# Optimization experiments

Measured on AMD Instinct MI355X. Metric: run time of the kernel, lower is better.

The kernel has to match this reference:

```python
import jax, jax.numpy as jnp
import numpy as np

N_HEAD = 16
QMIN, QMAX = 0.0, 255.0  # 8-bit asymmetric


def fake_quantize(x, scale, zp):
    # LearnableFakeQuantize (asymmetric, 8-bit) with straight-through round.
    q = x / scale + zp
    q = q + jax.lax.stop_gradient(jnp.round(q) - q)  # STE round
    q = jnp.clip(q, QMIN, QMAX)
    return (q - zp) * scale


def setup_inputs() -> dict:
    key = jax.random.key(0)
    ks = jax.random.split(key, 4)
    B, T, C = 2, 2048, 1024
    return {
        "hidden_states": jax.random.normal(ks[0], (B, T, C), jnp.float32),
        "W_attn": jax.random.normal(ks[1], (C, 3 * C), jnp.float32) * (1.0 / np.sqrt(C)),
        "b_attn": jnp.zeros((3 * C,), jnp.float32),
        "W_proj": jax.random.normal(ks[2], (C, C), jnp.float32) * (1.0 / np.sqrt(C)),
        "b_proj": jnp.zeros((C,), jnp.float32),
        "kv_scale": jnp.full((1,), 0.05, jnp.float32),
        "kv_zp": jnp.full((1,), 128.0, jnp.float32),
    }


def reference(hidden_states, W_attn, b_attn, W_proj, b_proj, kv_scale, kv_zp):
    B, T, C = hidden_states.shape
    H = N_HEAD
    D = C // H
    qkv = hidden_states @ W_attn + b_attn            # [B,T,3C]
    q, k, v = jnp.split(qkv, 3, axis=2)
    # [B,T,C] -> [B,H,T,D]
    q = q.reshape(B, T, H, D).transpose(0, 2, 1, 3)
    k = k.reshape(B, T, H, D).transpose(0, 2, 1, 3)
    v = v.reshape(B, T, H, D).transpose(0, 2, 1, 3)
    k = fake_quantize(k, kv_scale, kv_zp)
    v = fake_quantize(v, kv_scale, kv_zp)
    scores = jnp.einsum("bhqd,bhkd->bhqk", q, k) / jnp.sqrt(jnp.asarray(D, q.dtype))
    causal = jnp.tril(jnp.ones((T, T), bool))        # bias[:T,:T]
    scores = jnp.where(causal, scores, jnp.asarray(-jnp.inf, scores.dtype))
    attn = jax.nn.softmax(scores, axis=-1)
    out = jnp.einsum("bhqk,bhkd->bhqd", attn, v)     # [B,H,T,D]
    out = out.transpose(0, 2, 1, 3).reshape(B, T, C)
    return out @ W_proj + b_proj
```

## Files before the change

kernel.cpp:

```cpp
#include <hip/hip_runtime.h>
#include <math.h>

#define TB 2048
#define CC 1024
#define NH 16
#define HD 64

typedef __bf16 bf16x8 __attribute__((ext_vector_type(8)));
typedef __bf16 bf16x4 __attribute__((ext_vector_type(4)));
typedef float  f32x4  __attribute__((ext_vector_type(4)));

__device__ inline float exp2fast(float x) { return __builtin_amdgcn_exp2f(x); }

__device__ __forceinline__ void gl_lds16(const __bf16* g, __bf16* l) {
    __builtin_amdgcn_global_load_lds(
        (const __attribute__((address_space(1))) void*)g,
        (__attribute__((address_space(3))) void*)l, 16, 0, 0);
}

__global__ __launch_bounds__(256)
void prep_kernel(const float* __restrict__ hidden, __bf16* __restrict__ hb,
                 const float* __restrict__ Wa, __bf16* __restrict__ wat,
                 const float* __restrict__ Wp, __bf16* __restrict__ wpt)
{
    __shared__ __bf16 L[64][68];
    const int tid = threadIdx.x;
    const int bid = blockIdx.x;
    if (bid < 4096) {
        int i = (bid * 256 + tid) * 4;
        f32x4 v = *(const f32x4*)&hidden[i];
        bf16x4 o;
        o.x = (__bf16)v.x; o.y = (__bf16)v.y; o.z = (__bf16)v.z; o.w = (__bf16)v.w;
        *(bf16x4*)&hb[i] = o;
        return;
    }
    const float* src; __bf16* dst; int N, n0, k0;
    if (bid < 4096 + 768) {
        int t = bid - 4096;
        src = Wa; dst = wat; N = 3072;
        n0 = (t % 48) * 64; k0 = (t / 48) * 64;
    } else {
        int t = bid - 4864;
        src = Wp; dst = wpt; N = 1024;
        n0 = (t % 16) * 64; k0 = (t / 16) * 64;
    }
    #pragma unroll
    for (int i = 0; i < 4; i++) {
        int id = tid + i * 256;
        int r = id >> 4, c = (id & 15) * 4;
        f32x4 v = *(const f32x4*)&src[(size_t)(k0 + r) * N + n0 + c];
        bf16x4 o;
        o.x = (__bf16)v.x; o.y = (__bf16)v.y; o.z = (__bf16)v.z; o.w = (__bf16)v.w;
        *(bf16x4*)&L[r][c] = o;
    }
    __syncthreads();
    #pragma unroll
    for (int i = 0; i < 4; i++) {
        int id = tid + i * 256;
        int nr = id >> 4, kc = (id & 15) * 4;
        bf16x4 o;
        o.x = L[kc + 0][nr]; o.y = L[kc + 1][nr];
        o.z = L[kc + 2][nr]; o.w = L[kc + 3][nr];
        *(bf16x4*)&dst[(size_t)(n0 + nr) * 1024 + k0 + kc] = o;
    }
}

template<int BN, int MODE>
__global__ __launch_bounds__(256)
void gemm_bt(const __bf16* __restrict__ A, const __bf16* __restrict__ Bt,
             const float* __restrict__ bias,
             __bf16* __restrict__ o0, __bf16* __restrict__ o1,
             __bf16* __restrict__ o2, float* __restrict__ of,
             int M, int N, int K,
             const float* __restrict__ scp, const float* __restrict__ zpp)
{
    constexpr int NT = BN / 32;
    __shared__ __bf16 Asm[128][64];
    __shared__ __bf16 Bsm[BN][64];

    const int tid  = threadIdx.x;
    const int m0   = blockIdx.y * 128;
    const int n0   = blockIdx.x * BN;
    const int w    = tid >> 6, lane = tid & 63;
    const int wm   = (w & 1) * 64, wn = (w >> 1) * (BN / 2);
    const int r16  = lane & 15, quad = lane >> 4;
    const int srow = lane >> 3;
    const int scol = ((lane & 7) ^ srow) * 8;
    const int rsw  = r16 & 7;

    f32x4 acc[NT][4];
    #pragma unroll
    for (int i = 0; i < NT; i++)
        #pragma unroll
        for (int j = 0; j < 4; j++) acc[i][j] = 0.f;

    for (int k0 = 0; k0 < K; k0 += 64) {
        #pragma unroll
        for (int p = 0; p < 4; p++)
            gl_lds16(&A[(size_t)(m0 + w * 32 + p * 8 + srow) * K + k0 + scol],
                     &Asm[w * 32 + p * 8][0]);
        #pragma unroll
        for (int p = 0; p < BN / 32; p++)
            gl_lds16(&Bt[(size_t)(n0 + w * (BN / 4) + p * 8 + srow) * K + k0 + scol],
                     &Bsm[w * (BN / 4) + p * 8][0]);
        __syncthreads();

        #pragma unroll
        for (int ks = 0; ks < 2; ks++) {
            const int col = ((ks * 4 + quad) ^ rsw) * 8;
            bf16x8 af[4], bfr[NT];
            #pragma unroll
            for (int mt = 0; mt < 4; mt++)
                af[mt] = *(const bf16x8*)&Asm[wm + mt * 16 + r16][col];
            #pragma unroll
            for (int nt = 0; nt < NT; nt++)
                bfr[nt] = *(const bf16x8*)&Bsm[wn + nt * 16 + r16][col];
            #pragma unroll
            for (int nt = 0; nt < NT; nt++)
                #pragma unroll
                for (int mt = 0; mt < 4; mt++)
                    acc[nt][mt] = __builtin_amdgcn_mfma_f32_16x16x32_bf16(
                        bfr[nt], af[mt], acc[nt][mt], 0, 0, 0);
        }
        __syncthreads();
    }

    const float sc = scp[0];
    const float zp = zpp[0];

    #pragma unroll
    for (int nt = 0; nt < NT; nt++) {
        #pragma unroll
        for (int mt = 0; mt < 4; mt++) {
            int gm = m0 + wm + mt * 16 + r16;
            int gn = n0 + wn + nt * 16 + quad * 4;
            f32x4 val = acc[nt][mt] + *(const f32x4*)&bias[gn];
            if (MODE == 1) {
                *(f32x4*)&of[(size_t)gm * N + gn] = val;
            } else {
                int part = gn >> 10;
                int idx  = gn & 1023;
                int h = idx >> 6, d = idx & 63;
                int b = gm >> 11, t = gm & 2047;
                if (part == 0) {
                    size_t off = (((size_t)(b * NH + h)) * TB + t) * HD + d;
                    bf16x4 st;
                    #pragma unroll
                    for (int r = 0; r < 4; r++)
                        st[r] = (__bf16)(val[r] * 0.18033688f);
                    *(bf16x4*)&o0[off] = st;
                } else if (part == 1) {
                    size_t off = (((size_t)(b * NH + h)) * TB + t) * HD + d;
                    bf16x4 st;
                    #pragma unroll
                    for (int r = 0; r < 4; r++) {
                        float qv = val[r] / sc + zp;
                        qv = rintf(qv);
                        qv = fminf(fmaxf(qv, 0.f), 255.f);
                        st[r] = (__bf16)((qv - zp) * sc);
                    }
                    *(bf16x4*)&o1[off] = st;
                } else {
                    #pragma unroll
                    for (int r = 0; r < 4; r++) {
                        float qv = val[r] / sc + zp;
                        qv = rintf(qv);
                        qv = fminf(fmaxf(qv, 0.f), 255.f);
                        size_t offT = (((size_t)(b * NH + h)) * HD + d + r) * TB + t;
                        o2[offT] = (__bf16)((qv - zp) * sc);
                    }
                }
            }
        }
    }
}

__global__ __launch_bounds__(512, 4)
void attn_mfma(const __bf16* __restrict__ Q, const __bf16* __restrict__ Kg,
               const __bf16* __restrict__ VgT, __bf16* __restrict__ O)
{
    __shared__ alignas(16) __bf16 Ksm[2][64][64];
    __shared__ alignas(16) __bf16 Vsm[2][64][64];

    const int tid  = threadIdx.x;
    const int p    = blockIdx.x >> 5;
    const int bh   = blockIdx.x & 31;
    const int w    = tid >> 6, lane = tid & 63;
    const int wq   = w & 3;
    const int qt   = (w < 4) ? (31 - p) : p;
    const int ktmax = 31 - p;
    const int q0   = qt * 64;
    const int l15  = lane & 15, quad = lane >> 4;
    const int b    = bh >> 4, h = bh & 15;

    const int srow = tid >> 3;
    const int ssw  = ((tid & 7) ^ ((srow & 3) | (((srow >> 3) & 1) << 2))) * 8;

    const __bf16* Kbh = Kg  + (size_t)bh * TB * HD;
    const __bf16* Vbh = VgT + (size_t)bh * HD * TB;

    const __bf16* Qrow = Q + ((size_t)bh * TB + q0 + wq * 16 + l15) * HD;
    bf16x8 qf0 = *(const bf16x8*)&Qrow[quad * 8];
    bf16x8 qf1 = *(const bf16x8*)&Qrow[32 + quad * 8];

    const int rbase = (l15 >> 2) * 8 + (l15 & 3);
    const int fk   = (l15 & 3) | (((l15 >> 2) & 1) << 2);
    const int fv   = (l15 & 3) | (((l15 >> 3) & 1) << 2);
    const int kc0  = (quad ^ fk) * 8, kc1 = ((quad + 4) ^ fk) * 8;
    const int vc0  = (quad ^ fv) * 8, vc1 = ((quad + 4) ^ fv) * 8;

    bf16x8 af_l;
    {
        __bf16 v = (l15 == 0) ? (__bf16)1.0f : (__bf16)0.0f;
        #pragma unroll
        for (int j = 0; j < 8; j++) af_l[j] = v;
    }

    f32x4 acc_o[4], acc_l;
    #pragma unroll
    for (int nt = 0; nt < 4; nt++) acc_o[nt] = 0.f;
    acc_l = 0.f;
    float mrun = -3.0e38f;

    auto stage = [&](int buf, int kt) {
        gl_lds16(&Kbh[(size_t)(kt * 64 + srow) * HD + ssw], &Ksm[buf][w * 8][0]);
        gl_lds16(&Vbh[(size_t)srow * TB + kt * 64 + ssw],   &Vsm[buf][w * 8][0]);
    };

    stage(0, 0);
    __syncthreads();

    for (int kt = 0; kt <= ktmax; kt++) {
        const int cur = kt & 1;

        if (kt < ktmax) stage(cur ^ 1, kt + 1);

        if (kt <= qt) {
            const bool diag = (kt == qt);

            f32x4 s[4];
            #pragma unroll
            for (int nt = 0; nt < 4; nt++) s[nt] = 0.f;
            __builtin_amdgcn_s_setprio(1);
            #pragma unroll
            for (int nt = 0; nt < 4; nt++) {
                if (diag && (nt & 1) && wq < 2) continue;
                int row = rbase + (nt & 1) * 32 + ((nt >> 1) << 2);
                bf16x8 kf0 = *(const bf16x8*)&Ksm[cur][row][kc0];
                bf16x8 kf1 = *(const bf16x8*)&Ksm[cur][row][kc1];
                s[nt] = __builtin_amdgcn_mfma_f32_16x16x32_bf16(kf0, qf0, s[nt], 0, 0, 0);
                s[nt] = __builtin_amdgcn_mfma_f32_16x16x32_bf16(kf1, qf1, s[nt], 0, 0, 0);
            }
            __builtin_amdgcn_s_setprio(0);

            if (diag) {
                #pragma unroll
                for (int nt = 0; nt < 4; nt++) {
                    int koff = (nt & 1) * 32 + ((nt >> 1) << 2) + quad * 8;
                    #pragma unroll
                    for (int r = 0; r < 4; r++)
                        if (koff + r > wq * 16 + l15) s[nt][r] = -3.0e38f;
                }
            }

            float m0 = fmaxf(fmaxf(s[0][0], s[0][1]), fmaxf(s[0][2], s[0][3]));
            float m1 = fmaxf(fmaxf(s[1][0], s[1][1]), fmaxf(s[1][2], s[1][3]));
            float m2 = fmaxf(fmaxf(s[2][0], s[2][1]), fmaxf(s[2][2], s[2][3]));
            float m3 = fmaxf(fmaxf(s[3][0], s[3][1]), fmaxf(s[3][2], s[3][3]));
            float mx = fmaxf(fmaxf(m0, m1), fmaxf(m2, m3));
            mx = fmaxf(mx, __shfl_xor(mx, 16));
            mx = fmaxf(mx, __shfl_xor(mx, 32));

            if (__any((mx - mrun) > 8.0f)) {
                float mnew  = fmaxf(mrun, mx);
                float alpha = exp2fast(mrun - mnew);
                mrun = mnew;
                #pragma unroll
                for (int nt = 0; nt < 4; nt++)
                    #pragma unroll
                    for (int r = 0; r < 4; r++) acc_o[nt][r] *= alpha;
                acc_l[0] *= alpha;
            }

            float pv[4][4];
            #pragma unroll
            for (int nt = 0; nt < 4; nt++)
                #pragma unroll
                for (int r = 0; r < 4; r++) pv[nt][r] = exp2fast(s[nt][r] - mrun);

            bf16x8 pf0, pf1;
            #pragma unroll
            for (int j = 0; j < 4; j++) {
                pf0[j]     = (__bf16)pv[0][j];
                pf0[4 + j] = (__bf16)pv[2][j];
                pf1[j]     = (__bf16)pv[1][j];
                pf1[4 + j] = (__bf16)pv[3][j];
            }

            __builtin_amdgcn_s_setprio(1);
            acc_l = __builtin_amdgcn_mfma_f32_16x16x32_bf16(af_l, pf0, acc_l, 0, 0, 0);
            acc_l = __builtin_amdgcn_mfma_f32_16x16x32_bf16(af_l, pf1, acc_l, 0, 0, 0);

            #pragma unroll
            for (int nt = 0; nt < 4; nt++) {
                bf16x8 vf0 = *(const bf16x8*)&Vsm[cur][nt * 16 + l15][vc0];
                bf16x8 vf1 = *(const bf16x8*)&Vsm[cur][nt * 16 + l15][vc1];
                acc_o[nt] = __builtin_amdgcn_mfma_f32_16x16x32_bf16(vf0, pf0, acc_o[nt], 0, 0, 0);
                acc_o[nt] = __builtin_amdgcn_mfma_f32_16x16x32_bf16(vf1, pf1, acc_o[nt], 0, 0, 0);
            }
            __builtin_amdgcn_s_setprio(0);
        }

        __syncthreads();
    }

    float lall = __shfl(acc_l[0], l15);
    float inv  = 1.f / lall;
    size_t trow = (size_t)(b * TB) + q0 + wq * 16 + l15;
    #pragma unroll
    for (int nt = 0; nt < 4; nt++) {
        bf16x4 st;
        #pragma unroll
        for (int r = 0; r < 4; r++) st[r] = (__bf16)(acc_o[nt][r] * inv);
        *(bf16x4*)&O[trow * CC + h * HD + nt * 16 + quad * 4] = st;
    }
}

extern "C" void kernel_launch(void* const* d_in, const int* in_sizes, int n_in,
                              void* d_out, int out_size, void* d_ws, size_t ws_size,
                              hipStream_t stream) {
    (void)in_sizes; (void)n_in; (void)out_size; (void)ws_size;
    const float* hidden   = (const float*)d_in[0];
    const float* W_attn   = (const float*)d_in[1];
    const float* b_attn   = (const float*)d_in[2];
    const float* W_proj   = (const float*)d_in[3];
    const float* b_proj   = (const float*)d_in[4];
    const float* kv_scale = (const float*)d_in[5];
    const float* kv_zp    = (const float*)d_in[6];
    float* out = (float*)d_out;

    __bf16* hb  = (__bf16*)d_ws;
    __bf16* wat = hb  + (size_t)4096 * 1024;
    __bf16* wpt = wat + (size_t)3072 * 1024;
    __bf16* qws = wpt + (size_t)1024 * 1024;
    __bf16* kws = qws + (size_t)2 * NH * TB * HD;
    __bf16* vws = kws + (size_t)2 * NH * TB * HD;
    __bf16* ows = vws + (size_t)2 * NH * TB * HD;

    prep_kernel<<<5120, 256, 0, stream>>>(hidden, hb, W_attn, wat, W_proj, wpt);

    gemm_bt<128, 0><<<dim3(24, 32), 256, 0, stream>>>(
        hb, wat, b_attn, qws, kws, vws, nullptr, 4096, 3072, 1024, kv_scale, kv_zp);

    attn_mfma<<<dim3(16 * 32), 512, 0, stream>>>(qws, kws, vws, ows);

    gemm_bt<64, 1><<<dim3(16, 32), 256, 0, stream>>>(
        ows, wpt, b_proj, nullptr, nullptr, nullptr, out, 4096, 1024, 1024,
        kv_scale, kv_zp);
}
```

Baseline: 185.7 us.

## Stage transposed V epilogue through LDS and remap QKV GEMM blocks per XCD

```diff
diff --git a/kernel.cpp b/kernel.cpp
--- a/kernel.cpp
+++ b/kernel.cpp
@@ -79,8 +79,17 @@
     __shared__ __bf16 Bsm[BN][64];
 
     const int tid  = threadIdx.x;
-    const int m0   = blockIdx.y * 128;
-    const int n0   = blockIdx.x * BN;
+    int bx, by;
+    if constexpr (MODE == 0) {
+        int lid = blockIdx.y * 24 + blockIdx.x;
+        int xcd = lid & 7, li = lid >> 3;
+        bx = (xcd & 1) * 12 + (li % 12);
+        by = (xcd >> 1) * 8 + (li / 12);
+    } else {
+        bx = blockIdx.x; by = blockIdx.y;
+    }
+    const int m0   = by * 128;
+    const int n0   = bx * BN;
     const int w    = tid >> 6, lane = tid & 63;
     const int wm   = (w & 1) * 64, wn = (w >> 1) * (BN / 2);
     const int r16  = lane & 15, quad = lane >> 4;
@@ -127,6 +136,45 @@
 
     const float sc = scp[0];
     const float zp = zpp[0];
+
+    if constexpr (MODE == 0) {
+        if (n0 >= 2048) {
+            __bf16 (*Th)[64] = (w & 1) ? Bsm : Asm;
+            #pragma unroll
+            for (int nt = 0; nt < NT; nt++) {
+                #pragma unroll
+                for (int mt = 0; mt < 4; mt++) {
+                    f32x4 val = acc[nt][mt] +
+                        *(const f32x4*)&bias[n0 + wn + nt * 16 + quad * 4];
+                    int m_loc = mt * 16 + r16;
+                    #pragma unroll
+                    for (int r = 0; r < 4; r++) {
+                        float qv = val[r] / sc + zp;
+                        qv = rintf(qv);
+                        qv = fminf(fmaxf(qv, 0.f), 255.f);
+                        int n_l = wn + nt * 16 + quad * 4 + r;
+                        int col = (((m_loc >> 3) ^ (n_l & 7)) << 3) | (m_loc & 7);
+                        Th[n_l][col] = (__bf16)((qv - zp) * sc);
+                    }
+                }
+            }
+            __syncthreads();
+            const int bb    = m0 >> 11;
+            const int tbase = m0 & 2047;
+            const int vbase = bb * 1024 + (n0 - 2048);
+            #pragma unroll
+            for (int i = 0; i < 8; i++) {
+                int c = i * 256 + tid;
+                int n = c >> 4, j = c & 15;
+                const __bf16* Sh = (j >> 3) ? &Bsm[0][0] : &Asm[0][0];
+                int col = (((j & 7) ^ (n & 7)) << 3);
+                bf16x8 v = *(const bf16x8*)&Sh[n * 64 + col];
+                *(bf16x8*)&o2[(size_t)(vbase + n) * TB + tbase +
+                              (j >> 3) * 64 + (j & 7) * 8] = v;
+            }
+            return;
+        }
+    }
 
     #pragma unroll
     for (int nt = 0; nt < NT; nt++) {
@@ -142,16 +190,14 @@
                 int idx  = gn & 1023;
                 int h = idx >> 6, d = idx & 63;
                 int b = gm >> 11, t = gm & 2047;
+                size_t off = (((size_t)(b * NH + h)) * TB + t) * HD + d;
+                bf16x4 st;
                 if (part == 0) {
-                    size_t off = (((size_t)(b * NH + h)) * TB + t) * HD + d;
-                    bf16x4 st;
                     #pragma unroll
                     for (int r = 0; r < 4; r++)
                         st[r] = (__bf16)(val[r] * 0.18033688f);
                     *(bf16x4*)&o0[off] = st;
-                } else if (part == 1) {
-                    size_t off = (((size_t)(b * NH + h)) * TB + t) * HD + d;
-                    bf16x4 st;
+                } else {
                     #pragma unroll
                     for (int r = 0; r < 4; r++) {
                         float qv = val[r] / sc + zp;
@@ -160,15 +206,6 @@
                         st[r] = (__bf16)((qv - zp) * sc);
                     }
                     *(bf16x4*)&o1[off] = st;
-                } else {
-                    #pragma unroll
-                    for (int r = 0; r < 4; r++) {
-                        float qv = val[r] / sc + zp;
-                        qv = rintf(qv);
-                        qv = fminf(fmaxf(qv, 0.f), 255.f);
-                        size_t offT = (((size_t)(b * NH + h)) * HD + d + r) * TB + t;
-                        o2[offT] = (__bf16)((qv - zp) * sc);
-                    }
                 }
             }
         }
```

After: 192.5 us. +3.7%, slower.
